# Optimization experiments

Measured on AMD Instinct MI355X. Metric: run time of the kernel, lower is better.

The kernel has to match this reference:

```python
import jax, jax.numpy as jnp
import numpy as np

B, CIN, H, W = 16, 3, 256, 256
COUT = 64
K = 3          # kernel size
PAD = 1
KK = K * K     # 9 taps
EPS = 1e-5     # BatchNorm eps


def conv3x3(x, w, b=None):
    y = jax.lax.conv_general_dilated(
        x, w, window_strides=(1, 1), padding=[(PAD, PAD), (PAD, PAD)],
        dimension_numbers=("NCHW", "OIHW", "NCHW"))
    if b is not None:
        y = y + b[None, :, None, None]
    return y


def deform_sample(x, off):
    """Bilinear sampling at per-pixel learned offsets (mmcv DeformConv2d, deform_groups=1).
    x: [B,C,H,W], off: [B,2*KK,H,W] interleaved (dy,dx) per kernel tap.
    Returns sampled taps [B,KK,H,W,C]."""
    b, c, h, w = x.shape
    dy = off[:, 0::2]  # [B,KK,H,W]
    dx = off[:, 1::2]
    ky, kx = jnp.meshgrid(jnp.arange(K), jnp.arange(K), indexing="ij")
    ky = (ky.reshape(-1) - PAD).astype(x.dtype)  # tap row offsets: -1,0,1
    kx = (kx.reshape(-1) - PAD).astype(x.dtype)
    gy = jnp.arange(h, dtype=x.dtype)
    gx = jnp.arange(w, dtype=x.dtype)
    # absolute (float) sampling positions per tap
    py = gy[None, None, :, None] + ky[None, :, None, None] + dy  # [B,KK,H,W]
    px = gx[None, None, None, :] + kx[None, :, None, None] + dx
    y0 = jnp.floor(py)
    x0 = jnp.floor(px)
    ly = py - y0
    lx = px - x0
    hy = 1.0 - ly
    hx = 1.0 - lx
    xt = x.transpose(0, 2, 3, 1)  # [B,H,W,C] for channel-last gather
    bi = jnp.arange(b)[:, None, None, None]

    def corner(yi, xi, wgt):
        valid = ((yi >= 0) & (yi <= h - 1) & (xi >= 0) & (xi <= w - 1)).astype(x.dtype)
        yc = jnp.clip(yi, 0, h - 1).astype(jnp.int32)
        xc = jnp.clip(xi, 0, w - 1).astype(jnp.int32)
        return xt[bi, yc, xc] * (wgt * valid)[..., None]  # [B,KK,H,W,C]

    v = (corner(y0, x0, hy * hx)
         + corner(y0, x0 + 1.0, hy * lx)
         + corner(y0 + 1.0, x0, ly * hx)
         + corner(y0 + 1.0, x0 + 1.0, ly * lx))
    return v


def setup_inputs() -> dict:
    key = jax.random.key(0)
    ks = jax.random.split(key, 7)
    x = jax.random.normal(ks[0], (B, CIN, H, W), dtype=jnp.float32)
    # conv_offset: 3x3 conv -> 2*KK offset channels (zero-init in mmcv; use small random)
    w_off = jax.random.normal(ks[1], (2 * KK, CIN, K, K), dtype=jnp.float32) * 0.01
    b_off = jnp.zeros((2 * KK,), dtype=jnp.float32)
    fan = CIN * KK
    w_dcn = jax.random.normal(ks[2], (COUT, CIN, K, K), dtype=jnp.float32) / np.sqrt(fan)
    w_conv = jax.random.normal(ks[3], (COUT, CIN, K, K), dtype=jnp.float32) / np.sqrt(fan)
    b_conv = jax.random.normal(ks[4], (COUT,), dtype=jnp.float32) * 0.01
    gamma = jnp.ones((COUT,), dtype=jnp.float32)
    beta = jnp.zeros((COUT,), dtype=jnp.float32)
    return {"x": x, "w_off": w_off, "b_off": b_off, "w_dcn": w_dcn,
            "w_conv": w_conv, "b_conv": b_conv, "gamma": gamma, "beta": beta}


def reference(x, w_off, b_off, w_dcn, w_conv, b_conv, gamma, beta):
    off = conv3x3(x, w_off, b_off)              # [B,18,H,W]
    taps = deform_sample(x, off)                # [B,KK,H,W,CIN]
    wk = w_dcn.reshape(COUT, CIN, KK).transpose(0, 2, 1)  # [O,KK,C]
    x_dcn = jnp.einsum("bkhwc,okc->bohw", taps, wk)       # deform conv (bias=False)
    x_res = conv3x3(x, w_conv, b_conv)
    y = x_res + x_dcn
    # BatchNorm2d (training mode: batch statistics, biased var)
    mean = y.mean(axis=(0, 2, 3))
    var = y.var(axis=(0, 2, 3))
    yn = (y - mean[None, :, None, None]) * jax.lax.rsqrt(var[None, :, None, None] + EPS)
    yb = yn * gamma[None, :, None, None] + beta[None, :, None, None]
    return yb * jax.nn.sigmoid(yb)  # SiLU
```

## Files before the change

kernel.cpp:

```cpp
#include <hip/hip_runtime.h>
#include <hip/hip_bf16.h>
#include <math.h>

#define BB 16
#define COUTC 64
#define HH 256
#define WWD 256
#define PW 260
#define NBLK (BB*HH)
#define NBLK2 2048
#define NBLKW (NBLK*4)
#define NPIX (BB*HH*WWD)
#define YTOT ((size_t)NPIX*COUTC)

typedef __attribute__((ext_vector_type(8))) short short8;
typedef __attribute__((ext_vector_type(4))) float f32x4;
typedef __attribute__((ext_vector_type(4))) unsigned short us4;
typedef __attribute__((ext_vector_type(8))) unsigned short us8;

__device__ __forceinline__ unsigned short f2bf(float f) {
    __hip_bfloat16 h = __float2bfloat16(f);
    return __builtin_bit_cast(unsigned short, h);
}
__device__ __forceinline__ float bf2f(unsigned short u) {
    unsigned v = (unsigned)u << 16;
    return __builtin_bit_cast(float, v);
}

__global__ __launch_bounds__(256) void prep_kernel(
    const float* __restrict__ x,
    us4* __restrict__ xp)
{
    const int b  = blockIdx.x / PW;
    const int yr = blockIdx.x % PW - 2;
    const bool rok = (yr >= 0) && (yr < HH);
    const float* xb = x + (size_t)b * (3*HH*WWD) + (size_t)(rok ? yr : 0)*WWD;
    for (int cx = threadIdx.x; cx < PW; cx += 256) {
        const int xx = cx - 2;
        const bool ok = rok && (xx >= 0) && (xx < WWD);
        float f0 = ok ? xb[0*(HH*WWD) + xx] : 0.f;
        float f1 = ok ? xb[1*(HH*WWD) + xx] : 0.f;
        float f2 = ok ? xb[2*(HH*WWD) + xx] : 0.f;
        us4 v = { f2bf(f0), f2bf(f1), f2bf(f2), 0 };
// ... 5 lines not shown
    const float* __restrict__ w_dcn,
    const float* __restrict__ w_conv,
    const float* __restrict__ w_off,
    unsigned short* __restrict__ wTg,
    unsigned short* __restrict__ wOg)
{
    for (int e = threadIdx.x; e < 512; e += 256) {
        const int kc = e >> 6, n = e & 63;
        const float* wsrc = (kc < 4) ? w_conv : w_dcn;
        const int kb = (kc & 3) * 8;
        us8 v;
        #pragma unroll
        for (int j = 0; j < 8; ++j) {
            int kk = kb + j;
            v[j] = (kk < 27) ? f2bf(wsrc[n*27 + kk]) : (unsigned short)0;
        }
        *(us8*)(wTg + e*8) = v;
    }
    if (threadIdx.x < 128) {
        const int e = threadIdx.x;
        const int nt2 = e >> 6, l = e & 63;
        const int n = nt2*16 + (l & 15);
        const int kb = (l >> 4) * 8;
        us8 v;
        #pragma unroll
        for (int j = 0; j < 8; ++j) {
            int kk = kb + j;
            v[j] = (n < 18 && kk < 27) ? f2bf(w_off[n*27 + kk]) : (unsigned short)0;
        }
        *(us8*)(wOg + e*8) = v;
    }
}

__device__ __forceinline__ void load_xn3(const us4* __restrict__ xpb, int h, int w,
                                         us8 r8[3], us4 r4[3])
{
    #pragma unroll
    for (int dy = 0; dy < 3; ++dy) {
        const us4* p = xpb + (size_t)(h+1+dy)*PW + (w+1);
        r8[dy] = *(const us8*)p;
        r4[dy] = p[2];
    }
}

template<bool BF16Y>
__global__ __launch_bounds__(256, 3) void dcn_wave_kernel(
    const float* __restrict__ x,
    const us4* __restrict__ xp,
    const unsigned short* __restrict__ wTg,
    const unsigned short* __restrict__ wOg,
    const float* __restrict__ b_off,
    const float* __restrict__ b_conv,
    float* __restrict__ outf,
    unsigned short* __restrict__ yws,
    float* __restrict__ psum,
    float* __restrict__ psq)
{
    __shared__ __align__(16) char kbuf[32768];
    __shared__ __align__(16) unsigned short sofs[4*64*24];

    const int tid = threadIdx.x;
    const int bid = blockIdx.x;
    const int w = tid;
    const int l   = tid & 63;
    const int wv  = tid >> 6;
    const int g   = l >> 4;
    const int r15 = l & 15;
    char* kw = kbuf + wv*8192;
    unsigned short* so = sofs + wv*64*24;

    short8 bfr[2][4];
    #pragma unroll
    for (int ks = 0; ks < 2; ++ks)
        #pragma unroll
        for (int nt = 0; nt < 4; ++nt) {
            const int kc = ks*4 + g, n = nt*16 + r15;
            bfr[ks][nt] = *(const short8*)(wTg + (kc*64 + n)*8);
        }
    short8 wof[2];
    #pragma unroll
    for (int nt2 = 0; nt2 < 2; ++nt2)
        wof[nt2] = *(const short8*)(wOg + (nt2*64 + l)*8);

    int eff = bid;
    int swz = ((eff & 7) << 9) | (eff >> 3);
    int b = swz >> 8, h = swz & 255;
    const us4* xpb = xp + (size_t)b*PW*PW;
    us8 c8v[3]; us4 c4v[3];
    load_xn3(xpb, h, w, c8v, c4v);

    #pragma unroll
    for (int it = 0; it < 2; ++it) {
        const int eff_n = eff + NBLK2;
        const int swz_n = ((eff_n & 7) << 9) | ((eff_n >> 3) & 511);
        const int b_n = swz_n >> 8, h_n = swz_n & 255;
        const us4* xpb_n = xp + (size_t)b_n*PW*PW;

        {
            unsigned short u[32];
            #pragma unroll
            for (int c = 0; c < 3; ++c)
                #pragma unroll
                for (int ky = 0; ky < 3; ++ky)
                    #pragma unroll
                    for (int kx = 0; kx < 3; ++kx)
                        u[c*9 + ky*3 + kx] = (kx == 2) ? c4v[ky][c]
                                                       : c8v[ky][kx*4 + c];
            #pragma unroll
            for (int k = 27; k < 32; ++k) u[k] = 0;
            #pragma unroll
            for (int c8 = 0; c8 < 4; ++c8) {
                uint4 v;
                v.x = (unsigned)u[c8*8+0] | ((unsigned)u[c8*8+1] << 16);
                v.y = (unsigned)u[c8*8+2] | ((unsigned)u[c8*8+3] << 16);
                v.z = (unsigned)u[c8*8+4] | ((unsigned)u[c8*8+5] << 16);
                v.w = (unsigned)u[c8*8+6] | ((unsigned)u[c8*8+7] << 16);
                *(uint4*)(kw + l*128 + ((c8 ^ (l & 7)) << 4)) = v;
            }
        }

        f32x4 dacc[4][2];
        {
            short8 af0[4];
            #pragma unroll
            for (int mt = 0; mt < 4; ++mt) {
                int row = mt*16 + r15;
                af0[mt] = *(const short8*)(kw + row*128 + ((g ^ (row & 7)) << 4));
            }
            #pragma unroll
            for (int mt = 0; mt < 4; ++mt)
                #pragma unroll
                for (int nt2 = 0; nt2 < 2; ++nt2) {
                    dacc[mt][nt2] = (f32x4){0.f, 0.f, 0.f, 0.f};
                    dacc[mt][nt2] = __builtin_amdgcn_mfma_f32_16x16x32_bf16(
                        af0[mt], wof[nt2], dacc[mt][nt2], 0, 0, 0);
                }
        }

        #pragma unroll
        for (int mt = 0; mt < 4; ++mt)
            #pragma unroll
            for (int nt2 = 0; nt2 < 2; ++nt2) {
                if (nt2 == 1 && r15 >= 2) continue;
                #pragma unroll
                for (int r = 0; r < 4; ++r)
                    so[(mt*16 + g*4 + r)*24 + nt2*16 + r15] = f2bf(dacc[mt][nt2][r]);
            }

        us8 n8[3]; us4 n4[3];
        if (it == 0) load_xn3(xpb_n, h_n, w, n8, n4);

        float off[18];
        {
            us8 o0 = *(const us8*)(so + l*24);
            us8 o1 = *(const us8*)(so + l*24 + 8);
            us4 o2 = *(const us4*)(so + l*24 + 16);
            #pragma unroll
            for (int j = 0; j < 8; ++j)  off[j]   = bf2f(o0[j]) + b_off[j];
            #pragma unroll
            for (int j = 0; j < 8; ++j)  off[8+j] = bf2f(o1[j]) + b_off[8+j];
            off[16] = bf2f(o2[0]) + b_off[16];
            off[17] = bf2f(o2[1]) + b_off[17];
        }

        unsigned short ut[32];
        #pragma unroll
        for (int k = 0; k < 9; ++k) {
            const int ky = k / 3, kx = k % 3;
            float py = (float)(h + ky - 1) + off[2*k];
            float px = (float)(w + kx - 1) + off[2*k + 1];
            float y0f = floorf(py), x0f = floorf(px);
            float ly = py - y0f, lx = px - x0f;
            float hy = 1.f - ly, hx = 1.f - lx;
            int y0 = (int)y0f, x0 = (int)x0f;
            float t0, t1, t2;

            if (__builtin_expect(y0 >= -2 && y0 <= 256 && x0 >= -2 && x0 <= 256, 1)) {
                const us4* p0 = xpb + (size_t)(y0+2)*PW + (x0+2);
                us8 r0 = *(const us8*)p0;
                us8 r1 = *(const us8*)(p0 + PW);
                float w00 = hy*hx, w01 = hy*lx, w10 = ly*hx, w11 = ly*lx;
                t0 = w00*bf2f(r0[0]) + w01*bf2f(r0[4]) + w10*bf2f(r1[0]) + w11*bf2f(r1[4]);
                t1 = w00*bf2f(r0[1]) + w01*bf2f(r0[5]) + w10*bf2f(r1[1]) + w11*bf2f(r1[5]);
                t2 = w00*bf2f(r0[2]) + w01*bf2f(r0[6]) + w10*bf2f(r1[2]) + w11*bf2f(r1[6]);
            } else {
                int y1 = y0 + 1, x1 = x0 + 1;
                bool vy0 = (y0 >= 0) && (y0 < HH);
                bool vy1 = (y1 >= 0) && (y1 < HH);
                bool vx0 = (x0 >= 0) && (x0 < WWD);
                bool vx1 = (x1 >= 0) && (x1 < WWD);
                float w00 = (vy0 && vx0) ? hy*hx : 0.f;
                float w01 = (vy0 && vx1) ? hy*lx : 0.f;
                float w10 = (vy1 && vx0) ? ly*hx : 0.f;
                float w11 = (vy1 && vx1) ? ly*lx : 0.f;
                int yc0 = min(max(y0, 0), HH-1),  yc1 = min(max(y1, 0), HH-1);
                int xc0 = min(max(x0, 0), WWD-1), xc1 = min(max(x1, 0), WWD-1);
                const float* xb = x + (size_t)b * (3*HH*WWD);
                const float* x0p = xb;
                t0 = w00*x0p[yc0*WWD+xc0] + w01*x0p[yc0*WWD+xc1]
                   + w10*x0p[yc1*WWD+xc0] + w11*x0p[yc1*WWD+xc1];
                const float* x1p = xb + HH*WWD;
                t1 = w00*x1p[yc0*WWD+xc0] + w01*x1p[yc0*WWD+xc1]
                   + w10*x1p[yc1*WWD+xc0] + w11*x1p[yc1*WWD+xc1];
                const float* x2p = xb + 2*HH*WWD;
                t2 = w00*x2p[yc0*WWD+xc0] + w01*x2p[yc0*WWD+xc1]
                   + w10*x2p[yc1*WWD+xc0] + w11*x2p[yc1*WWD+xc1];
            }
            ut[0*9 + k] = f2bf(t0);
            ut[1*9 + k] = f2bf(t1);
            ut[2*9 + k] = f2bf(t2);
        }
        #pragma unroll
        for (int k = 27; k < 32; ++k) ut[k] = 0;

        #pragma unroll
        for (int c8 = 4; c8 < 8; ++c8) {
            const int j0 = (c8 - 4) * 8;
            uint4 v;
            v.x = (unsigned)ut[j0+0] | ((unsigned)ut[j0+1] << 16);
            v.y = (unsigned)ut[j0+2] | ((unsigned)ut[j0+3] << 16);
            v.z = (unsigned)ut[j0+4] | ((unsigned)ut[j0+5] << 16);
            v.w = (unsigned)ut[j0+6] | ((unsigned)ut[j0+7] << 16);
            *(uint4*)(kw + l*128 + ((c8 ^ (l & 7)) << 4)) = v;
        }

        short8 a0[4], a1[4];
        #pragma unroll
        for (int mt = 0; mt < 4; ++mt) {
            int row = mt*16 + r15;
            a0[mt] = *(const short8*)(kw + row*128 + (( g      ^ (row & 7)) << 4));
            a1[mt] = *(const short8*)(kw + row*128 + (((4 + g) ^ (row & 7)) << 4));
        }

        #pragma unroll
        for (int nt = 0; nt < 4; ++nt) {
            f32x4 acc[4];
            #pragma unroll
            for (int mt = 0; mt < 4; ++mt)
                acc[mt] = (f32x4){0.f, 0.f, 0.f, 0.f};
            #pragma unroll
            for (int mt = 0; mt < 4; ++mt)
                acc[mt] = __builtin_amdgcn_mfma_f32_16x16x32_bf16(a0[mt], bfr[0][nt], acc[mt], 0, 0, 0);
            #pragma unroll
            for (int mt = 0; mt < 4; ++mt)
                acc[mt] = __builtin_amdgcn_mfma_f32_16x16x32_bf16(a1[mt], bfr[1][nt], acc[mt], 0, 0, 0);

            const float bcv = b_conv[nt*16 + r15];
            float s = 0.f, s2 = 0.f;
            const size_t base = ((size_t)(b*64 + nt*16 + r15) << 16)
                              + (size_t)h*256 + wv*64 + g*4;
            #pragma unroll
            for (int mt = 0; mt < 4; ++mt) {
                f32x4 v = acc[mt];
                float ox = v.x + bcv, oy = v.y + bcv, oz = v.z + bcv, ow = v.w + bcv;
                s += ox + oy + oz + ow;
                s2 = fmaf(ox, ox, s2); s2 = fmaf(oy, oy, s2);
                s2 = fmaf(oz, oz, s2); s2 = fmaf(ow, ow, s2);
                if (BF16Y) {
                    us4 pv = { f2bf(ox), f2bf(oy), f2bf(oz), f2bf(ow) };
                    *(us4*)(yws + base + mt*16) = pv;
                } else {
                    float4 pv = { ox, oy, oz, ow };
                    *(float4*)(outf + base + mt*16) = pv;
                }
            }
            s  += __shfl_xor(s, 16);  s  += __shfl_xor(s, 32);
            s2 += __shfl_xor(s2, 16); s2 += __shfl_xor(s2, 32);
            if (l < 16) {
                psum[(nt*16 + l)*NBLKW + swz*4 + wv] = s;
                psq [(nt*16 + l)*NBLKW + swz*4 + wv] = s2;
            }
        }

        if (it == 0) {
            eff = eff_n; swz = swz_n; b = b_n; h = h_n; xpb = xpb_n;
            #pragma unroll
            for (int dy = 0; dy < 3; ++dy) { c8v[dy] = n8[dy]; c4v[dy] = n4[dy]; }
        }
    }
}

__global__ __launch_bounds__(256) void bn_stats_kernel(
    const float* __restrict__ psum,
    const float* __restrict__ psq,
    const float* __restrict__ gamma,
    const float* __restrict__ beta,
    float* __restrict__ ss)
{
    __shared__ float rs[256], rq[256];
    const int ch = blockIdx.x, tid = threadIdx.x;
    float s = 0.f, s2 = 0.f;
    for (int j = tid; j < NBLKW; j += 256) {
        s  += psum[ch*NBLKW + j];
        s2 += psq [ch*NBLKW + j];
    }
    rs[tid] = s; rq[tid] = s2;
    __syncthreads();
    for (int st = 128; st > 0; st >>= 1) {
        if (tid < st) { rs[tid] += rs[tid + st]; rq[tid] += rq[tid + st]; }
        __syncthreads();
    }
    if (tid == 0) {
        const float N = (float)NPIX;
        float mean = rs[0] / N;
        float var  = rq[0] / N - mean*mean;
        float rstd = rsqrtf(var + 1e-5f);
        float sc   = gamma[ch] * rstd;
        ss[ch]      = sc;
        ss[64 + ch] = beta[ch] - mean * sc;
    }
}

// ... 49 lines not shown
        z = fmaf(v.w, a, t); v.w = z / (1.f + __expf(-z));
        y4[i] = v;
    }
}

extern "C" void kernel_launch(void* const* d_in, const int* in_sizes, int n_in,
                              void* d_out, int out_size, void* d_ws, size_t ws_size,
                              hipStream_t stream) {
    const float* x      = (const float*)d_in[0];
    const float* w_off  = (const float*)d_in[1];
    const float* b_off  = (const float*)d_in[2];
    const float* w_dcn  = (const float*)d_in[3];
    const float* w_conv = (const float*)d_in[4];
    const float* b_conv = (const float*)d_in[5];
    const float* gamma  = (const float*)d_in[6];
    const float* beta   = (const float*)d_in[7];
    float* out = (float*)d_out;

    const size_t yBytes    = YTOT * 2;
    const size_t xpBytes   = (size_t)BB*PW*PW*8;
    const size_t wtgBytes  = 8192 + 2048;
    const size_t statBytes = 2*(size_t)64*NBLKW*4 + 512;

    if (ws_size >= yBytes + xpBytes + wtgBytes + statBytes) {
        unsigned short* yws = (unsigned short*)d_ws;
        us4*            xpp = (us4*)((char*)d_ws + yBytes);
        unsigned short* wTg = (unsigned short*)((char*)d_ws + yBytes + xpBytes);
        unsigned short* wOg = wTg + 4096;
        float* psum = (float*)((char*)d_ws + yBytes + xpBytes + wtgBytes);
        float* psq  = psum + (size_t)64*NBLKW;
        float* ss   = psq  + (size_t)64*NBLKW;
        prep_kernel<<<BB*PW, 256, 0, stream>>>(x, xpp);
        wtg_kernel<<<1, 256, 0, stream>>>(w_dcn, w_conv, w_off, wTg, wOg);
        dcn_wave_kernel<true><<<NBLK2, 256, 0, stream>>>(
            x, xpp, wTg, wOg, b_off, b_conv, nullptr, yws, psum, psq);
        bn_stats_kernel<<<64, 256, 0, stream>>>(psum, psq, gamma, beta, ss);
        bn_silu_bf16_kernel<<<2048, 256, 0, stream>>>(yws, out, ss);
    } else {
        us4*            xpp = (us4*)d_ws;
        unsigned short* wTg = (unsigned short*)((char*)d_ws + xpBytes);
        unsigned short* wOg = wTg + 4096;
        float* psum = (float*)((char*)d_ws + xpBytes + wtgBytes);
        float* psq  = psum + (size_t)64*NBLKW;
        float* ss   = psq  + (size_t)64*NBLKW;
        prep_kernel<<<BB*PW, 256, 0, stream>>>(x, xpp);
        wtg_kernel<<<1, 256, 0, stream>>>(w_dcn, w_conv, w_off, wTg, wOg);
        dcn_wave_kernel<false><<<NBLK2, 256, 0, stream>>>(
            x, xpp, wTg, wOg, b_off, b_conv, out, nullptr, psum, psq);
        bn_stats_kernel<<<64, 256, 0, stream>>>(psum, psq, gamma, beta, ss);
        bn_silu_kernel<<<2048, 256, 0, stream>>>(out, ss);
    }
}
```

Baseline: 184.8 us.

## Batch all deformable tap gathers upfront, one row per block, drop fp32 fallback

The kernel now handles one image row per block over NBLK blocks, replacing the two-row loop that software-prefetched the next row's neighbourhood. It first computes offsets, weights and clamped addresses for all nine taps, then issues all eighteen gathers together so they are in flight at once. The out-of-window fallback now reads the padded bf16 buffer instead of the fp32 input, and index maths uses 32-bit unsigned arithmetic. Launch bounds drop from 3 to 2 blocks per SU, trading occupancy and extra registers for more memory-level parallelism per thread.

New measurement: 187.8 us. Within noise of the previous version (+1.6%).

```diff
diff --git a/kernel.cpp b/kernel.cpp
--- a/kernel.cpp
+++ b/kernel.cpp
@@ -8,7 +8,6 @@
 #define WWD 256
 #define PW 260
 #define NBLK (BB*HH)
-#define NBLK2 2048
 #define NBLKW (NBLK*4)
 #define NPIX (BB*HH*WWD)
 #define YTOT ((size_t)NPIX*COUTC)
@@ -80,20 +79,8 @@
     }
 }
 
-__device__ __forceinline__ void load_xn3(const us4* __restrict__ xpb, int h, int w,
-                                         us8 r8[3], us4 r4[3])
-{
-    #pragma unroll
-    for (int dy = 0; dy < 3; ++dy) {
-        const us4* p = xpb + (size_t)(h+1+dy)*PW + (w+1);
-        r8[dy] = *(const us8*)p;
-        r4[dy] = p[2];
-    }
-}
-
 template<bool BF16Y>
-__global__ __launch_bounds__(256, 3) void dcn_wave_kernel(
-    const float* __restrict__ x,
+__global__ __launch_bounds__(256, 2) void dcn_wave_kernel(
     const us4* __restrict__ xp,
     const unsigned short* __restrict__ wTg,
     const unsigned short* __restrict__ wOg,
@@ -109,6 +96,9 @@
 
     const int tid = threadIdx.x;
     const int bid = blockIdx.x;
+    const int swz = ((bid & 7) << 9) | (bid >> 3);
+    const int b = swz >> 8;
+    const int h = swz & 255;
     const int w = tid;
     const int l   = tid & 63;
     const int wv  = tid >> 6;
@@ -117,6 +107,16 @@
     char* kw = kbuf + wv*8192;
     unsigned short* so = sofs + wv*64*24;
 
+    const us4* xpb = xp + (unsigned)b*(PW*PW);
+
+    us8 c8v[3]; us4 c4v[3];
+    #pragma unroll
+    for (int dy = 0; dy < 3; ++dy) {
+        const us4* p = xpb + (unsigned)((h+1+dy)*PW + (w+1));
+        c8v[dy] = *(const us8*)p;
+        c4v[dy] = p[2];
+    }
+
     short8 bfr[2][4];
     #pragma unroll
     for (int ks = 0; ks < 2; ++ks)
@@ -130,108 +130,116 @@
     for (int nt2 = 0; nt2 < 2; ++nt2)
         wof[nt2] = *(const short8*)(wOg + (nt2*64 + l)*8);
 
-    int eff = bid;
-    int swz = ((eff & 7) << 9) | (eff >> 3);
-    int b = swz >> 8, h = swz & 255;
-    const us4* xpb = xp + (size_t)b*PW*PW;
-    us8 c8v[3]; us4 c4v[3];
-    load_xn3(xpb, h, w, c8v, c4v);
-
-    #pragma unroll
-    for (int it = 0; it < 2; ++it) {
-        const int eff_n = eff + NBLK2;
-        const int swz_n = ((eff_n & 7) << 9) | ((eff_n >> 3) & 511);
-        const int b_n = swz_n >> 8, h_n = swz_n & 255;
-        const us4* xpb_n = xp + (size_t)b_n*PW*PW;
-
-        {
-            unsigned short u[32];
+    {
+        unsigned short u[32];
+        #pragma unroll
+        for (int c = 0; c < 3; ++c)
             #pragma unroll
-            for (int c = 0; c < 3; ++c)
+            for (int ky = 0; ky < 3; ++ky)
                 #pragma unroll
-                for (int ky = 0; ky < 3; ++ky)
-                    #pragma unroll
-                    for (int kx = 0; kx < 3; ++kx)
-                        u[c*9 + ky*3 + kx] = (kx == 2) ? c4v[ky][c]
-                                                       : c8v[ky][kx*4 + c];
-            #pragma unroll
-            for (int k = 27; k < 32; ++k) u[k] = 0;
-            #pragma unroll
-            for (int c8 = 0; c8 < 4; ++c8) {
-                uint4 v;
-                v.x = (unsigned)u[c8*8+0] | ((unsigned)u[c8*8+1] << 16);
-                v.y = (unsigned)u[c8*8+2] | ((unsigned)u[c8*8+3] << 16);
-                v.z = (unsigned)u[c8*8+4] | ((unsigned)u[c8*8+5] << 16);
-                v.w = (unsigned)u[c8*8+6] | ((unsigned)u[c8*8+7] << 16);
-                *(uint4*)(kw + l*128 + ((c8 ^ (l & 7)) << 4)) = v;
-            }
-        }
-
-        f32x4 dacc[4][2];
-        {
-            short8 af0[4];
-            #pragma unroll
-            for (int mt = 0; mt < 4; ++mt) {
-                int row = mt*16 + r15;
-                af0[mt] = *(const short8*)(kw + row*128 + ((g ^ (row & 7)) << 4));
-            }
-            #pragma unroll
-            for (int mt = 0; mt < 4; ++mt)
-                #pragma unroll
-                for (int nt2 = 0; nt2 < 2; ++nt2) {
-                    dacc[mt][nt2] = (f32x4){0.f, 0.f, 0.f, 0.f};
-                    dacc[mt][nt2] = __builtin_amdgcn_mfma_f32_16x16x32_bf16(
-                        af0[mt], wof[nt2], dacc[mt][nt2], 0, 0, 0);
-                }
-        }
-
+                for (int kx = 0; kx < 3; ++kx)
+                    u[c*9 + ky*3 + kx] = (kx == 2) ? c4v[ky][c]
+                                                   : c8v[ky][kx*4 + c];
+        #pragma unroll
+        for (int k = 27; k < 32; ++k) u[k] = 0;
+        #pragma unroll
+        for (int c8 = 0; c8 < 4; ++c8) {
+            uint4 v;
+            v.x = (unsigned)u[c8*8+0] | ((unsigned)u[c8*8+1] << 16);
+            v.y = (unsigned)u[c8*8+2] | ((unsigned)u[c8*8+3] << 16);
+            v.z = (unsigned)u[c8*8+4] | ((unsigned)u[c8*8+5] << 16);
+            v.w = (unsigned)u[c8*8+6] | ((unsigned)u[c8*8+7] << 16);
+            *(uint4*)(kw + l*128 + ((c8 ^ (l & 7)) << 4)) = v;
+        }
+    }
+
+    f32x4 dacc[4][2];
+    {
+        short8 af0[4];
+        #pragma unroll
+        for (int mt = 0; mt < 4; ++mt) {
+            int row = mt*16 + r15;
+            af0[mt] = *(const short8*)(kw + row*128 + ((g ^ (row & 7)) << 4));
+        }
         #pragma unroll
         for (int mt = 0; mt < 4; ++mt)
             #pragma unroll
             for (int nt2 = 0; nt2 < 2; ++nt2) {
-                if (nt2 == 1 && r15 >= 2) continue;
-                #pragma unroll
-                for (int r = 0; r < 4; ++r)
-                    so[(mt*16 + g*4 + r)*24 + nt2*16 + r15] = f2bf(dacc[mt][nt2][r]);
+                dacc[mt][nt2] = (f32x4){0.f, 0.f, 0.f, 0.f};
+                dacc[mt][nt2] = __builtin_amdgcn_mfma_f32_16x16x32_bf16(
+                    af0[mt], wof[nt2], dacc[mt][nt2], 0, 0, 0);
             }
-
-        us8 n8[3]; us4 n4[3];
-        if (it == 0) load_xn3(xpb_n, h_n, w, n8, n4);
-
-        float off[18];
-        {
-            us8 o0 = *(const us8*)(so + l*24);
-            us8 o1 = *(const us8*)(so + l*24 + 8);
-            us4 o2 = *(const us4*)(so + l*24 + 16);
+    }
+
+    #pragma unroll
+    for (int mt = 0; mt < 4; ++mt)
+        #pragma unroll
+        for (int nt2 = 0; nt2 < 2; ++nt2) {
+            if (nt2 == 1 && r15 >= 2) continue;
             #pragma unroll
-            for (int j = 0; j < 8; ++j)  off[j]   = bf2f(o0[j]) + b_off[j];
-            #pragma unroll
-            for (int j = 0; j < 8; ++j)  off[8+j] = bf2f(o1[j]) + b_off[8+j];
-            off[16] = bf2f(o2[0]) + b_off[16];
-            off[17] = bf2f(o2[1]) + b_off[17];
-        }
-
-        unsigned short ut[32];
-        #pragma unroll
-        for (int k = 0; k < 9; ++k) {
-            const int ky = k / 3, kx = k % 3;
-            float py = (float)(h + ky - 1) + off[2*k];
-            float px = (float)(w + kx - 1) + off[2*k + 1];
-            float y0f = floorf(py), x0f = floorf(px);
-            float ly = py - y0f, lx = px - x0f;
-            float hy = 1.f - ly, hx = 1.f - lx;
-            int y0 = (int)y0f, x0 = (int)x0f;
-            float t0, t1, t2;
-
-            if (__builtin_expect(y0 >= -2 && y0 <= 256 && x0 >= -2 && x0 <= 256, 1)) {
-                const us4* p0 = xpb + (size_t)(y0+2)*PW + (x0+2);
-                us8 r0 = *(const us8*)p0;
-                us8 r1 = *(const us8*)(p0 + PW);
-                float w00 = hy*hx, w01 = hy*lx, w10 = ly*hx, w11 = ly*lx;
-                t0 = w00*bf2f(r0[0]) + w01*bf2f(r0[4]) + w10*bf2f(r1[0]) + w11*bf2f(r1[4]);
-                t1 = w00*bf2f(r0[1]) + w01*bf2f(r0[5]) + w10*bf2f(r1[1]) + w11*bf2f(r1[5]);
-                t2 = w00*bf2f(r0[2]) + w01*bf2f(r0[6]) + w10*bf2f(r1[2]) + w11*bf2f(r1[6]);
-            } else {
+            for (int r = 0; r < 4; ++r)
+                so[(mt*16 + g*4 + r)*24 + nt2*16 + r15] = f2bf(dacc[mt][nt2][r]);
+        }
+
+    float off[18];
+    {
+        us8 o0 = *(const us8*)(so + l*24);
+        us8 o1 = *(const us8*)(so + l*24 + 8);
+        us4 o2 = *(const us4*)(so + l*24 + 16);
+        #pragma unroll
+        for (int j = 0; j < 8; ++j)  off[j]   = bf2f(o0[j]) + b_off[j];
+        #pragma unroll
+        for (int j = 0; j < 8; ++j)  off[8+j] = bf2f(o1[j]) + b_off[8+j];
+        off[16] = bf2f(o2[0]) + b_off[16];
+        off[17] = bf2f(o2[1]) + b_off[17];
+    }
+
+    int   o32[9];
+    float W00[9], W01[9], W10[9], W11[9];
+    unsigned inwm = 0;
+    #pragma unroll
+    for (int k = 0; k < 9; ++k) {
+        const int ky = k / 3, kx = k % 3;
+        float py = (float)(h + ky - 1) + off[2*k];
+        float px = (float)(w + kx - 1) + off[2*k + 1];
+        float y0f = floorf(py), x0f = floorf(px);
+        float ly = py - y0f, lx = px - x0f;
+        float hy = 1.f - ly, hx = 1.f - lx;
+        int y0 = (int)y0f, x0 = (int)x0f;
+        bool inw = (y0 >= -2) & (y0 <= 256) & (x0 >= -2) & (x0 <= 256);
+        inwm |= (unsigned)inw << k;
+        int y0c = min(max(y0, -2), 256), x0c = min(max(x0, -2), 256);
+        o32[k] = (y0c + 2)*PW + (x0c + 2);
+        W00[k] = hy*hx; W01[k] = hy*lx; W10[k] = ly*hx; W11[k] = ly*lx;
+    }
+
+    us8 ra[9], rb[9];
+    #pragma unroll
+    for (int k = 0; k < 9; ++k) {
+        const us4* p0 = xpb + (unsigned)o32[k];
+        ra[k] = *(const us8*)p0;
+        rb[k] = *(const us8*)(p0 + PW);
+    }
+
+    unsigned short ut[32];
+    #pragma unroll
+    for (int k = 0; k < 9; ++k) {
+        float t0 = W00[k]*bf2f(ra[k][0]) + W01[k]*bf2f(ra[k][4])
+                 + W10[k]*bf2f(rb[k][0]) + W11[k]*bf2f(rb[k][4]);
+        float t1 = W00[k]*bf2f(ra[k][1]) + W01[k]*bf2f(ra[k][5])
+                 + W10[k]*bf2f(rb[k][1]) + W11[k]*bf2f(rb[k][5]);
+        float t2 = W00[k]*bf2f(ra[k][2]) + W01[k]*bf2f(ra[k][6])
+                 + W10[k]*bf2f(rb[k][2]) + W11[k]*bf2f(rb[k][6]);
+
+        if (__builtin_expect(__any(((inwm >> k) & 1u) == 0u), 0)) {
+            if (!((inwm >> k) & 1u)) {
+                const int ky = k / 3, kx = k % 3;
+                float py = (float)(h + ky - 1) + off[2*k];
+                float px = (float)(w + kx - 1) + off[2*k + 1];
+                float y0f = floorf(py), x0f = floorf(px);
+                float ly = py - y0f, lx = px - x0f;
+                float hy = 1.f - ly, hx = 1.f - lx;
+                int y0 = (int)y0f, x0 = (int)x0f;
                 int y1 = y0 + 1, x1 = x0 + 1;
                 bool vy0 = (y0 >= 0) && (y0 < HH);
                 bool vy1 = (y1 >= 0) && (y1 < HH);
@@ -243,87 +251,78 @@
                 float w11 = (vy1 && vx1) ? ly*lx : 0.f;
                 int yc0 = min(max(y0, 0), HH-1),  yc1 = min(max(y1, 0), HH-1);
                 int xc0 = min(max(x0, 0), WWD-1), xc1 = min(max(x1, 0), WWD-1);
-                const float* xb = x + (size_t)b * (3*HH*WWD);
-                const float* x0p = xb;
-                t0 = w00*x0p[yc0*WWD+xc0] + w01*x0p[yc0*WWD+xc1]
-                   + w10*x0p[yc1*WWD+xc0] + w11*x0p[yc1*WWD+xc1];
-                const float* x1p = xb + HH*WWD;
-                t1 = w00*x1p[yc0*WWD+xc0] + w01*x1p[yc0*WWD+xc1]
-                   + w10*x1p[yc1*WWD+xc0] + w11*x1p[yc1*WWD+xc1];
-                const float* x2p = xb + 2*HH*WWD;
-                t2 = w00*x2p[yc0*WWD+xc0] + w01*x2p[yc0*WWD+xc1]
-                   + w10*x2p[yc1*WWD+xc0] + w11*x2p[yc1*WWD+xc1];
+                us4 q00 = xpb[(unsigned)((yc0+2)*PW + xc0+2)];
+                us4 q01 = xpb[(unsigned)((yc0+2)*PW + xc1+2)];
+                us4 q10 = xpb[(unsigned)((yc1+2)*PW + xc0+2)];
+                us4 q11 = xpb[(unsigned)((yc1+2)*PW + xc1+2)];
+                t0 = w00*bf2f(q00[0]) + w01*bf2f(q01[0]) + w10*bf2f(q10[0]) + w11*bf2f(q11[0]);
+                t1 = w00*bf2f(q00[1]) + w01*bf2f(q01[1]) + w10*bf2f(q10[1]) + w11*bf2f(q11[1]);
+                t2 = w00*bf2f(q00[2]) + w01*bf2f(q01[2]) + w10*bf2f(q10[2]) + w11*bf2f(q11[2]);
             }
-            ut[0*9 + k] = f2bf(t0);
-            ut[1*9 + k] = f2bf(t1);
-            ut[2*9 + k] = f2bf(t2);
-        }
-        #pragma unroll
-        for (int k = 27; k < 32; ++k) ut[k] = 0;
-
-        #pragma unroll
-        for (int c8 = 4; c8 < 8; ++c8) {
-            const int j0 = (c8 - 4) * 8;
-            uint4 v;
-            v.x = (unsigned)ut[j0+0] | ((unsigned)ut[j0+1] << 16);
-            v.y = (unsigned)ut[j0+2] | ((unsigned)ut[j0+3] << 16);
-            v.z = (unsigned)ut[j0+4] | ((unsigned)ut[j0+5] << 16);
-            v.w = (unsigned)ut[j0+6] | ((unsigned)ut[j0+7] << 16);
-            *(uint4*)(kw + l*128 + ((c8 ^ (l & 7)) << 4)) = v;
-        }
-
-        short8 a0[4], a1[4];
+        }
+        ut[0*9 + k] = f2bf(t0);
+        ut[1*9 + k] = f2bf(t1);
+        ut[2*9 + k] = f2bf(t2);
+    }
+    #pragma unroll
+    for (int k = 27; k < 32; ++k) ut[k] = 0;
+
+    #pragma unroll
+    for (int c8 = 4; c8 < 8; ++c8) {
+        const int j0 = (c8 - 4) * 8;
+        uint4 v;
+        v.x = (unsigned)ut[j0+0] | ((unsigned)ut[j0+1] << 16);
+        v.y = (unsigned)ut[j0+2] | ((unsigned)ut[j0+3] << 16);
+        v.z = (unsigned)ut[j0+4] | ((unsigned)ut[j0+5] << 16);
+        v.w = (unsigned)ut[j0+6] | ((unsigned)ut[j0+7] << 16);
+        *(uint4*)(kw + l*128 + ((c8 ^ (l & 7)) << 4)) = v;
+    }
+
+    short8 a0[4], a1[4];
+    #pragma unroll
+    for (int mt = 0; mt < 4; ++mt) {
+        int row = mt*16 + r15;
+        a0[mt] = *(const short8*)(kw + row*128 + (( g      ^ (row & 7)) << 4));
+        a1[mt] = *(const short8*)(kw + row*128 + (((4 + g) ^ (row & 7)) << 4));
+    }
+
+    #pragma unroll
+    for (int nt = 0; nt < 4; ++nt) {
+        f32x4 acc[4];
+        #pragma unroll
+        for (int mt = 0; mt < 4; ++mt)
+            acc[mt] = (f32x4){0.f, 0.f, 0.f, 0.f};
+        #pragma unroll
+        for (int mt = 0; mt < 4; ++mt)
+            acc[mt] = __builtin_amdgcn_mfma_f32_16x16x32_bf16(a0[mt], bfr[0][nt], acc[mt], 0, 0, 0);
+        #pragma unroll
+        for (int mt = 0; mt < 4; ++mt)
+            acc[mt] = __builtin_amdgcn_mfma_f32_16x16x32_bf16(a1[mt], bfr[1][nt], acc[mt], 0, 0, 0);
+
+        const float bcv = b_conv[nt*16 + r15];
+        float s = 0.f, s2 = 0.f;
+        const unsigned base = ((unsigned)(b*64 + nt*16 + r15) << 16)
+                            + (unsigned)(h*256 + wv*64 + g*4);
         #pragma unroll
         for (int mt = 0; mt < 4; ++mt) {
-            int row = mt*16 + r15;
-            a0[mt] = *(const short8*)(kw + row*128 + (( g      ^ (row & 7)) << 4));
-            a1[mt] = *(const short8*)(kw + row*128 + (((4 + g) ^ (row & 7)) << 4));
-        }
-
-        #pragma unroll
-        for (int nt = 0; nt < 4; ++nt) {
-            f32x4 acc[4];
-            #pragma unroll
-            for (int mt = 0; mt < 4; ++mt)
-                acc[mt] = (f32x4){0.f, 0.f, 0.f, 0.f};
-            #pragma unroll
-            for (int mt = 0; mt < 4; ++mt)
-                acc[mt] = __builtin_amdgcn_mfma_f32_16x16x32_bf16(a0[mt], bfr[0][nt], acc[mt], 0, 0, 0);
-            #pragma unroll
-            for (int mt = 0; mt < 4; ++mt)
-                acc[mt] = __builtin_amdgcn_mfma_f32_16x16x32_bf16(a1[mt], bfr[1][nt], acc[mt], 0, 0, 0);
-
-            const float bcv = b_conv[nt*16 + r15];
-            float s = 0.f, s2 = 0.f;
-            const size_t base = ((size_t)(b*64 + nt*16 + r15) << 16)
-                              + (size_t)h*256 + wv*64 + g*4;
-            #pragma unroll
-            for (int mt = 0; mt < 4; ++mt) {
-                f32x4 v = acc[mt];
-                float ox = v.x + bcv, oy = v.y + bcv, oz = v.z + bcv, ow = v.w + bcv;
-                s += ox + oy + oz + ow;
-                s2 = fmaf(ox, ox, s2); s2 = fmaf(oy, oy, s2);
-                s2 = fmaf(oz, oz, s2); s2 = fmaf(ow, ow, s2);
-                if (BF16Y) {
-                    us4 pv = { f2bf(ox), f2bf(oy), f2bf(oz), f2bf(ow) };
-                    *(us4*)(yws + base + mt*16) = pv;
-                } else {
-                    float4 pv = { ox, oy, oz, ow };
-                    *(float4*)(outf + base + mt*16) = pv;
-                }
+            f32x4 v = acc[mt];
+            float ox = v.x + bcv, oy = v.y + bcv, oz = v.z + bcv, ow = v.w + bcv;
+            s += ox + oy + oz + ow;
+            s2 = fmaf(ox, ox, s2); s2 = fmaf(oy, oy, s2);
+            s2 = fmaf(oz, oz, s2); s2 = fmaf(ow, ow, s2);
+            if (BF16Y) {
+                us4 pv = { f2bf(ox), f2bf(oy), f2bf(oz), f2bf(ow) };
+                *(us4*)(yws + base + mt*16) = pv;
+            } else {
+                float4 pv = { ox, oy, oz, ow };
+                *(float4*)(outf + base + mt*16) = pv;
             }
-            s  += __shfl_xor(s, 16);  s  += __shfl_xor(s, 32);
-            s2 += __shfl_xor(s2, 16); s2 += __shfl_xor(s2, 32);
-            if (l < 16) {
-                psum[(nt*16 + l)*NBLKW + swz*4 + wv] = s;
-                psq [(nt*16 + l)*NBLKW + swz*4 + wv] = s2;
-            }
-        }
-
-        if (it == 0) {
-            eff = eff_n; swz = swz_n; b = b_n; h = h_n; xpb = xpb_n;
-            #pragma unroll
-            for (int dy = 0; dy < 3; ++dy) { c8v[dy] = n8[dy]; c4v[dy] = n4[dy]; }
+        }
+        s  += __shfl_xor(s, 16);  s  += __shfl_xor(s, 32);
+        s2 += __shfl_xor(s2, 16); s2 += __shfl_xor(s2, 32);
+        if (l < 16) {
+            psum[(unsigned)((nt*16 + l)*NBLKW + swz*4 + wv)] = s;
+            psq [(unsigned)((nt*16 + l)*NBLKW + swz*4 + wv)] = s2;
         }
     }
 }
@@ -441,8 +440,8 @@
         float* ss   = psq  + (size_t)64*NBLKW;
         prep_kernel<<<BB*PW, 256, 0, stream>>>(x, xpp);
         wtg_kernel<<<1, 256, 0, stream>>>(w_dcn, w_conv, w_off, wTg, wOg);
-        dcn_wave_kernel<true><<<NBLK2, 256, 0, stream>>>(
-            x, xpp, wTg, wOg, b_off, b_conv, nullptr, yws, psum, psq);
+        dcn_wave_kernel<true><<<NBLK, 256, 0, stream>>>(
+            xpp, wTg, wOg, b_off, b_conv, nullptr, yws, psum, psq);
         bn_stats_kernel<<<64, 256, 0, stream>>>(psum, psq, gamma, beta, ss);
         bn_silu_bf16_kernel<<<2048, 256, 0, stream>>>(yws, out, ss);
     } else {
@@ -454,8 +453,8 @@
         float* ss   = psq  + (size_t)64*NBLKW;
         prep_kernel<<<BB*PW, 256, 0, stream>>>(x, xpp);
         wtg_kernel<<<1, 256, 0, stream>>>(w_dcn, w_conv, w_off, wTg, wOg);
-        dcn_wave_kernel<false><<<NBLK2, 256, 0, stream>>>(
-            x, xpp, wTg, wOg, b_off, b_conv, out, nullptr, psum, psq);
+        dcn_wave_kernel<false><<<NBLK, 256, 0, stream>>>(
+            xpp, wTg, wOg, b_off, b_conv, out, nullptr, psum, psq);
         bn_stats_kernel<<<64, 256, 0, stream>>>(psum, psq, gamma, beta, ss);
         bn_silu_kernel<<<2048, 256, 0, stream>>>(out, ss);
     }
```

## Software-pipeline two row tiles per block with interleaved gather loads

Applied to the files above, without the earlier changes.

Restructures the deform-conv kernel so each block processes its two rows in an interleaved schedule. Both rows' offset convs run first, then the second row's gather loads are issued while the first row's bilinear math and main MFMA run. This hides global gather latency. The out-of-bounds fallback that read unpadded x is replaced by clamping coordinates into the padded buffer, and 32-bit offsets replace size_t addressing. LDS doubles and launch bounds drop to 2 blocks per CU to make room for the extra live state, which costs occupancy.

New measurement: 181.7 us. Within noise of the previous version (-1.7%).

```diff
diff --git a/kernel.cpp b/kernel.cpp
--- a/kernel.cpp
+++ b/kernel.cpp
@@ -85,15 +85,197 @@
 {
     #pragma unroll
     for (int dy = 0; dy < 3; ++dy) {
-        const us4* p = xpb + (size_t)(h+1+dy)*PW + (w+1);
+        const us4* p = xpb + (unsigned)((h+1+dy)*PW + (w+1));
         r8[dy] = *(const us8*)p;
         r4[dy] = p[2];
     }
 }
 
+__device__ __forceinline__ void pack_xn_half(char* kw, int l,
+                                             const us8 c8v[3], const us4 c4v[3])
+{
+    unsigned short u[32];
+    #pragma unroll
+    for (int c = 0; c < 3; ++c)
+        #pragma unroll
+        for (int ky = 0; ky < 3; ++ky)
+            #pragma unroll
+            for (int kx = 0; kx < 3; ++kx)
+                u[c*9 + ky*3 + kx] = (kx == 2) ? c4v[ky][c] : c8v[ky][kx*4 + c];
+    #pragma unroll
+    for (int k = 27; k < 32; ++k) u[k] = 0;
+    #pragma unroll
+    for (int c8 = 0; c8 < 4; ++c8) {
+        uint4 v;
+        v.x = (unsigned)u[c8*8+0] | ((unsigned)u[c8*8+1] << 16);
+        v.y = (unsigned)u[c8*8+2] | ((unsigned)u[c8*8+3] << 16);
+        v.z = (unsigned)u[c8*8+4] | ((unsigned)u[c8*8+5] << 16);
+        v.w = (unsigned)u[c8*8+6] | ((unsigned)u[c8*8+7] << 16);
+        *(uint4*)(kw + l*128 + ((c8 ^ (l & 7)) << 4)) = v;
+    }
+}
+
+__device__ __forceinline__ void off_conv_mfma(const char* kw, int g, int r15,
+                                              const short8 wof[2], f32x4 dacc[4][2])
+{
+    short8 af0[4];
+    #pragma unroll
+    for (int mt = 0; mt < 4; ++mt) {
+        int row = mt*16 + r15;
+        af0[mt] = *(const short8*)(kw + row*128 + ((g ^ (row & 7)) << 4));
+    }
+    #pragma unroll
+    for (int mt = 0; mt < 4; ++mt)
+        #pragma unroll
+        for (int nt2 = 0; nt2 < 2; ++nt2) {
+            dacc[mt][nt2] = (f32x4){0.f, 0.f, 0.f, 0.f};
+            dacc[mt][nt2] = __builtin_amdgcn_mfma_f32_16x16x32_bf16(
+                af0[mt], wof[nt2], dacc[mt][nt2], 0, 0, 0);
+        }
+}
+
+__device__ __forceinline__ void redist_read_off(unsigned short* so, int l, int g,
+                                                int r15, const f32x4 dacc[4][2],
+                                                const float* __restrict__ b_off,
+                                                float off[18])
+{
+    #pragma unroll
+    for (int mt = 0; mt < 4; ++mt)
+        #pragma unroll
+        for (int nt2 = 0; nt2 < 2; ++nt2) {
+            if (nt2 == 1 && r15 >= 2) continue;
+            #pragma unroll
+            for (int r = 0; r < 4; ++r)
+                so[(mt*16 + g*4 + r)*24 + nt2*16 + r15] = f2bf(dacc[mt][nt2][r]);
+        }
+    us8 o0 = *(const us8*)(so + l*24);
+    us8 o1 = *(const us8*)(so + l*24 + 8);
+    us4 o2 = *(const us4*)(so + l*24 + 16);
+    #pragma unroll
+    for (int j = 0; j < 8; ++j)  off[j]   = bf2f(o0[j]) + b_off[j];
+    #pragma unroll
+    for (int j = 0; j < 8; ++j)  off[8+j] = bf2f(o1[j]) + b_off[8+j];
+    off[16] = bf2f(o2[0]) + b_off[16];
+    off[17] = bf2f(o2[1]) + b_off[17];
+}
+
+__device__ __forceinline__ void tap_addrs(int h, int w, const float off[18],
+                                          int o32[9], float W00[9], float W01[9],
+                                          float W10[9], float W11[9])
+{
+    #pragma unroll
+    for (int k = 0; k < 9; ++k) {
+        const int ky = k / 3, kx = k % 3;
+        float py = (float)(h + ky - 1) + off[2*k];
+        float px = (float)(w + kx - 1) + off[2*k + 1];
+        float y0f = floorf(py), x0f = floorf(px);
+        float ly = py - y0f, lx = px - x0f;
+        float hy = 1.f - ly, hx = 1.f - lx;
+        int y0 = min(max((int)y0f, -2), 256);
+        int x0 = min(max((int)x0f, -2), 256);
+        o32[k] = (y0 + 2)*PW + (x0 + 2);
+        W00[k] = hy*hx; W01[k] = hy*lx; W10[k] = ly*hx; W11[k] = ly*lx;
+    }
+}
+
+__device__ __forceinline__ void tap_loads(const us4* __restrict__ xpb,
+                                          const int o32[9], us8 ra[9], us8 rb[9])
+{
+    #pragma unroll
+    for (int k = 0; k < 9; ++k) {
+        const us4* p0 = xpb + (unsigned)o32[k];
+        ra[k] = *(const us8*)p0;
+        rb[k] = *(const us8*)(p0 + PW);
+    }
+}
+
+__device__ __forceinline__ void tap_math_pack(char* kw, int l,
+                                              const float W00[9], const float W01[9],
+                                              const float W10[9], const float W11[9],
+                                              const us8 ra[9], const us8 rb[9])
+{
+    unsigned short ut[32];
+    #pragma unroll
+    for (int k = 0; k < 9; ++k) {
+        #pragma unroll
+        for (int c = 0; c < 3; ++c) {
+            float t = W00[k]*bf2f(ra[k][c])   + W01[k]*bf2f(ra[k][4+c])
+                    + W10[k]*bf2f(rb[k][c])   + W11[k]*bf2f(rb[k][4+c]);
+            ut[c*9 + k] = f2bf(t);
+        }
+    }
+    #pragma unroll
+    for (int k = 27; k < 32; ++k) ut[k] = 0;
+    #pragma unroll
+    for (int c8 = 4; c8 < 8; ++c8) {
+        const int j0 = (c8 - 4) * 8;
+        uint4 v;
+        v.x = (unsigned)ut[j0+0] | ((unsigned)ut[j0+1] << 16);
+        v.y = (unsigned)ut[j0+2] | ((unsigned)ut[j0+3] << 16);
+        v.z = (unsigned)ut[j0+4] | ((unsigned)ut[j0+5] << 16);
+        v.w = (unsigned)ut[j0+6] | ((unsigned)ut[j0+7] << 16);
+        *(uint4*)(kw + l*128 + ((c8 ^ (l & 7)) << 4)) = v;
+    }
+}
+
 template<bool BF16Y>
-__global__ __launch_bounds__(256, 3) void dcn_wave_kernel(
-    const float* __restrict__ x,
+__device__ __forceinline__ void main_mfma_epilogue(
+    const char* kw, int l, int wv, int g, int r15,
+    const short8 bfr[2][4], const float* __restrict__ b_conv,
+    int swz, int b, int h,
+    float* __restrict__ outf, unsigned short* __restrict__ yws,
+    float* __restrict__ psum, float* __restrict__ psq)
+{
+    short8 a0[4], a1[4];
+    #pragma unroll
+    for (int mt = 0; mt < 4; ++mt) {
+        int row = mt*16 + r15;
+        a0[mt] = *(const short8*)(kw + row*128 + (( g      ^ (row & 7)) << 4));
+        a1[mt] = *(const short8*)(kw + row*128 + (((4 + g) ^ (row & 7)) << 4));
+    }
+    #pragma unroll
+    for (int nt = 0; nt < 4; ++nt) {
+        f32x4 acc[4];
+        #pragma unroll
+        for (int mt = 0; mt < 4; ++mt)
+            acc[mt] = (f32x4){0.f, 0.f, 0.f, 0.f};
+        #pragma unroll
+        for (int mt = 0; mt < 4; ++mt)
+            acc[mt] = __builtin_amdgcn_mfma_f32_16x16x32_bf16(a0[mt], bfr[0][nt], acc[mt], 0, 0, 0);
+        #pragma unroll
+        for (int mt = 0; mt < 4; ++mt)
+            acc[mt] = __builtin_amdgcn_mfma_f32_16x16x32_bf16(a1[mt], bfr[1][nt], acc[mt], 0, 0, 0);
+
+        const float bcv = b_conv[nt*16 + r15];
+        float s = 0.f, s2 = 0.f;
+        const size_t base = ((size_t)(b*64 + nt*16 + r15) << 16)
+                          + (size_t)h*256 + wv*64 + g*4;
+        #pragma unroll
+        for (int mt = 0; mt < 4; ++mt) {
+            f32x4 v = acc[mt];
+            float ox = v.x + bcv, oy = v.y + bcv, oz = v.z + bcv, ow = v.w + bcv;
+            s += ox + oy + oz + ow;
+            s2 = fmaf(ox, ox, s2); s2 = fmaf(oy, oy, s2);
+            s2 = fmaf(oz, oz, s2); s2 = fmaf(ow, ow, s2);
+            if (BF16Y) {
+                us4 pv = { f2bf(ox), f2bf(oy), f2bf(oz), f2bf(ow) };
+                *(us4*)(yws + base + mt*16) = pv;
+            } else {
+                float4 pv = { ox, oy, oz, ow };
+                *(float4*)(outf + base + mt*16) = pv;
+            }
+        }
+        s  += __shfl_xor(s, 16);  s  += __shfl_xor(s, 32);
+        s2 += __shfl_xor(s2, 16); s2 += __shfl_xor(s2, 32);
+        if (l < 16) {
+            psum[(nt*16 + l)*NBLKW + swz*4 + wv] = s;
+            psq [(nt*16 + l)*NBLKW + swz*4 + wv] = s2;
+        }
+    }
+}
+
+template<bool BF16Y>
+__global__ __launch_bounds__(256, 2) void dcn_wave_kernel(
     const us4* __restrict__ xp,
     const unsigned short* __restrict__ wTg,
     const unsigned short* __restrict__ wOg,
@@ -104,8 +286,8 @@
     float* __restrict__ psum,
     float* __restrict__ psq)
 {
-    __shared__ __align__(16) char kbuf[32768];
-    __shared__ __align__(16) unsigned short sofs[4*64*24];
+    __shared__ __align__(16) char kbuf[65536];
+    __shared__ __align__(16) unsigned short sofs[6144];
 
     const int tid = threadIdx.x;
     const int bid = blockIdx.x;
@@ -114,8 +296,17 @@
     const int wv  = tid >> 6;
     const int g   = l >> 4;
     const int r15 = l & 15;
-    char* kw = kbuf + wv*8192;
+    char* kw0 = kbuf + wv*8192;
+    char* kw1 = kbuf + (4 + wv)*8192;
     unsigned short* so = sofs + wv*64*24;
+
+    const int eff0 = bid,         eff1 = bid + NBLK2;
+    const int swz0 = ((eff0 & 7) << 9) | (eff0 >> 3);
+    const int swz1 = ((eff1 & 7) << 9) | ((eff1 >> 3) & 511);
+    const int b0 = swz0 >> 8, h0 = swz0 & 255;
+    const int b1 = swz1 >> 8, h1 = swz1 & 255;
+    const us4* xpb0 = xp + (size_t)b0*PW*PW;
+    const us4* xpb1 = xp + (size_t)b1*PW*PW;
 
     short8 bfr[2][4];
     #pragma unroll
@@ -130,202 +321,41 @@
     for (int nt2 = 0; nt2 < 2; ++nt2)
         wof[nt2] = *(const short8*)(wOg + (nt2*64 + l)*8);
 
-    int eff = bid;
-    int swz = ((eff & 7) << 9) | (eff >> 3);
-    int b = swz >> 8, h = swz & 255;
-    const us4* xpb = xp + (size_t)b*PW*PW;
-    us8 c8v[3]; us4 c4v[3];
-    load_xn3(xpb, h, w, c8v, c4v);
-
-    #pragma unroll
-    for (int it = 0; it < 2; ++it) {
-        const int eff_n = eff + NBLK2;
-        const int swz_n = ((eff_n & 7) << 9) | ((eff_n >> 3) & 511);
-        const int b_n = swz_n >> 8, h_n = swz_n & 255;
-        const us4* xpb_n = xp + (size_t)b_n*PW*PW;
-
-        {
-            unsigned short u[32];
-            #pragma unroll
-            for (int c = 0; c < 3; ++c)
-                #pragma unroll
-                for (int ky = 0; ky < 3; ++ky)
-                    #pragma unroll
-                    for (int kx = 0; kx < 3; ++kx)
-                        u[c*9 + ky*3 + kx] = (kx == 2) ? c4v[ky][c]
-                                                       : c8v[ky][kx*4 + c];
-            #pragma unroll
-            for (int k = 27; k < 32; ++k) u[k] = 0;
-            #pragma unroll
-            for (int c8 = 0; c8 < 4; ++c8) {
-                uint4 v;
-                v.x = (unsigned)u[c8*8+0] | ((unsigned)u[c8*8+1] << 16);
-                v.y = (unsigned)u[c8*8+2] | ((unsigned)u[c8*8+3] << 16);
-                v.z = (unsigned)u[c8*8+4] | ((unsigned)u[c8*8+5] << 16);
-                v.w = (unsigned)u[c8*8+6] | ((unsigned)u[c8*8+7] << 16);
-                *(uint4*)(kw + l*128 + ((c8 ^ (l & 7)) << 4)) = v;
-            }
-        }
-
-        f32x4 dacc[4][2];
-        {
-            short8 af0[4];
-            #pragma unroll
-            for (int mt = 0; mt < 4; ++mt) {
-                int row = mt*16 + r15;
-                af0[mt] = *(const short8*)(kw + row*128 + ((g ^ (row & 7)) << 4));
-            }
-            #pragma unroll
-            for (int mt = 0; mt < 4; ++mt)
-                #pragma unroll
-                for (int nt2 = 0; nt2 < 2; ++nt2) {
-                    dacc[mt][nt2] = (f32x4){0.f, 0.f, 0.f, 0.f};
-                    dacc[mt][nt2] = __builtin_amdgcn_mfma_f32_16x16x32_bf16(
-                        af0[mt], wof[nt2], dacc[mt][nt2], 0, 0, 0);
-                }
-        }
-
-        #pragma unroll
-        for (int mt = 0; mt < 4; ++mt)
-            #pragma unroll
-            for (int nt2 = 0; nt2 < 2; ++nt2) {
-                if (nt2 == 1 && r15 >= 2) continue;
-                #pragma unroll
-                for (int r = 0; r < 4; ++r)
-                    so[(mt*16 + g*4 + r)*24 + nt2*16 + r15] = f2bf(dacc[mt][nt2][r]);
-            }
-
-        us8 n8[3]; us4 n4[3];
-        if (it == 0) load_xn3(xpb_n, h_n, w, n8, n4);
-
-        float off[18];
-        {
-            us8 o0 = *(const us8*)(so + l*24);
-            us8 o1 = *(const us8*)(so + l*24 + 8);
-            us4 o2 = *(const us4*)(so + l*24 + 16);
-            #pragma unroll
-            for (int j = 0; j < 8; ++j)  off[j]   = bf2f(o0[j]) + b_off[j];
-            #pragma unroll
-            for (int j = 0; j < 8; ++j)  off[8+j] = bf2f(o1[j]) + b_off[8+j];
-            off[16] = bf2f(o2[0]) + b_off[16];
-            off[17] = bf2f(o2[1]) + b_off[17];
-        }
-
-        unsigned short ut[32];
-        #pragma unroll
-        for (int k = 0; k < 9; ++k) {
-            const int ky = k / 3, kx = k % 3;
-            float py = (float)(h + ky - 1) + off[2*k];
-            float px = (float)(w + kx - 1) + off[2*k + 1];
-            float y0f = floorf(py), x0f = floorf(px);
-            float ly = py - y0f, lx = px - x0f;
-            float hy = 1.f - ly, hx = 1.f - lx;
-            int y0 = (int)y0f, x0 = (int)x0f;
-            float t0, t1, t2;
-
-            if (__builtin_expect(y0 >= -2 && y0 <= 256 && x0 >= -2 && x0 <= 256, 1)) {
-                const us4* p0 = xpb + (size_t)(y0+2)*PW + (x0+2);
-                us8 r0 = *(const us8*)p0;
-                us8 r1 = *(const us8*)(p0 + PW);
-                float w00 = hy*hx, w01 = hy*lx, w10 = ly*hx, w11 = ly*lx;
-                t0 = w00*bf2f(r0[0]) + w01*bf2f(r0[4]) + w10*bf2f(r1[0]) + w11*bf2f(r1[4]);
-                t1 = w00*bf2f(r0[1]) + w01*bf2f(r0[5]) + w10*bf2f(r1[1]) + w11*bf2f(r1[5]);
-                t2 = w00*bf2f(r0[2]) + w01*bf2f(r0[6]) + w10*bf2f(r1[2]) + w11*bf2f(r1[6]);
-            } else {
-                int y1 = y0 + 1, x1 = x0 + 1;
-                bool vy0 = (y0 >= 0) && (y0 < HH);
-                bool vy1 = (y1 >= 0) && (y1 < HH);
-                bool vx0 = (x0 >= 0) && (x0 < WWD);
-                bool vx1 = (x1 >= 0) && (x1 < WWD);
-                float w00 = (vy0 && vx0) ? hy*hx : 0.f;
-                float w01 = (vy0 && vx1) ? hy*lx : 0.f;
-                float w10 = (vy1 && vx0) ? ly*hx : 0.f;
-                float w11 = (vy1 && vx1) ? ly*lx : 0.f;
-                int yc0 = min(max(y0, 0), HH-1),  yc1 = min(max(y1, 0), HH-1);
-                int xc0 = min(max(x0, 0), WWD-1), xc1 = min(max(x1, 0), WWD-1);
-                const float* xb = x + (size_t)b * (3*HH*WWD);
-                const float* x0p = xb;
-                t0 = w00*x0p[yc0*WWD+xc0] + w01*x0p[yc0*WWD+xc1]
-                   + w10*x0p[yc1*WWD+xc0] + w11*x0p[yc1*WWD+xc1];
-                const float* x1p = xb + HH*WWD;
-                t1 = w00*x1p[yc0*WWD+xc0] + w01*x1p[yc0*WWD+xc1]
-                   + w10*x1p[yc1*WWD+xc0] + w11*x1p[yc1*WWD+xc1];
-                const float* x2p = xb + 2*HH*WWD;
-                t2 = w00*x2p[yc0*WWD+xc0] + w01*x2p[yc0*WWD+xc1]
-                   + w10*x2p[yc1*WWD+xc0] + w11*x2p[yc1*WWD+xc1];
-            }
-            ut[0*9 + k] = f2bf(t0);
-            ut[1*9 + k] = f2bf(t1);
-            ut[2*9 + k] = f2bf(t2);
-        }
-        #pragma unroll
-        for (int k = 27; k < 32; ++k) ut[k] = 0;
-
-        #pragma unroll
-        for (int c8 = 4; c8 < 8; ++c8) {
-            const int j0 = (c8 - 4) * 8;
-            uint4 v;
-            v.x = (unsigned)ut[j0+0] | ((unsigned)ut[j0+1] << 16);
-            v.y = (unsigned)ut[j0+2] | ((unsigned)ut[j0+3] << 16);
-            v.z = (unsigned)ut[j0+4] | ((unsigned)ut[j0+5] << 16);
-            v.w = (unsigned)ut[j0+6] | ((unsigned)ut[j0+7] << 16);
-            *(uint4*)(kw + l*128 + ((c8 ^ (l & 7)) << 4)) = v;
-        }
-
-        short8 a0[4], a1[4];
-        #pragma unroll
-        for (int mt = 0; mt < 4; ++mt) {
-            int row = mt*16 + r15;
-            a0[mt] = *(const short8*)(kw + row*128 + (( g      ^ (row & 7)) << 4));
-            a1[mt] = *(const short8*)(kw + row*128 + (((4 + g) ^ (row & 7)) << 4));
-        }
-
-        #pragma unroll
-        for (int nt = 0; nt < 4; ++nt) {
-            f32x4 acc[4];
-            #pragma unroll
-            for (int mt = 0; mt < 4; ++mt)
-                acc[mt] = (f32x4){0.f, 0.f, 0.f, 0.f};
-            #pragma unroll
-            for (int mt = 0; mt < 4; ++mt)
-                acc[mt] = __builtin_amdgcn_mfma_f32_16x16x32_bf16(a0[mt], bfr[0][nt], acc[mt], 0, 0, 0);
-            #pragma unroll
-            for (int mt = 0; mt < 4; ++mt)
-                acc[mt] = __builtin_amdgcn_mfma_f32_16x16x32_bf16(a1[mt], bfr[1][nt], acc[mt], 0, 0, 0);
-
-            const float bcv = b_conv[nt*16 + r15];
-            float s = 0.f, s2 = 0.f;
-            const size_t base = ((size_t)(b*64 + nt*16 + r15) << 16)
-                              + (size_t)h*256 + wv*64 + g*4;
-            #pragma unroll
-            for (int mt = 0; mt < 4; ++mt) {
-                f32x4 v = acc[mt];
-                float ox = v.x + bcv, oy = v.y + bcv, oz = v.z + bcv, ow = v.w + bcv;
-                s += ox + oy + oz + ow;
-                s2 = fmaf(ox, ox, s2); s2 = fmaf(oy, oy, s2);
-                s2 = fmaf(oz, oz, s2); s2 = fmaf(ow, ow, s2);
-                if (BF16Y) {
-                    us4 pv = { f2bf(ox), f2bf(oy), f2bf(oz), f2bf(ow) };
-                    *(us4*)(yws + base + mt*16) = pv;
-                } else {
-                    float4 pv = { ox, oy, oz, ow };
-                    *(float4*)(outf + base + mt*16) = pv;
-                }
-            }
-            s  += __shfl_xor(s, 16);  s  += __shfl_xor(s, 32);
-            s2 += __shfl_xor(s2, 16); s2 += __shfl_xor(s2, 32);
-            if (l < 16) {
-                psum[(nt*16 + l)*NBLKW + swz*4 + wv] = s;
-                psq [(nt*16 + l)*NBLKW + swz*4 + wv] = s2;
-            }
-        }
-
-        if (it == 0) {
-            eff = eff_n; swz = swz_n; b = b_n; h = h_n; xpb = xpb_n;
-            #pragma unroll
-            for (int dy = 0; dy < 3; ++dy) { c8v[dy] = n8[dy]; c4v[dy] = n4[dy]; }
-        }
-    }
+    us8 c8v0[3]; us4 c4v0[3];
+    us8 c8v1[3]; us4 c4v1[3];
+    load_xn3(xpb0, h0, w, c8v0, c4v0);
+    load_xn3(xpb1, h1, w, c8v1, c4v1);
+
+    pack_xn_half(kw0, l, c8v0, c4v0);
+    pack_xn_half(kw1, l, c8v1, c4v1);
+
+    f32x4 dacc0[4][2], dacc1[4][2];
+    off_conv_mfma(kw0, g, r15, wof, dacc0);
+    off_conv_mfma(kw1, g, r15, wof, dacc1);
+
+    float off0[18], off1[18];
+    redist_read_off(so, l, g, r15, dacc0, b_off, off0);
+    redist_read_off(so, l, g, r15, dacc1, b_off, off1);
+
+    int o32_0[9]; float W00_0[9], W01_0[9], W10_0[9], W11_0[9];
+    tap_addrs(h0, w, off0, o32_0, W00_0, W01_0, W10_0, W11_0);
+    us8 ra0[9], rb0[9];
+    tap_loads(xpb0, o32_0, ra0, rb0);
+
+    int o32_1[9]; float W00_1[9], W01_1[9], W10_1[9], W11_1[9];
+    tap_addrs(h1, w, off1, o32_1, W00_1, W01_1, W10_1, W11_1);
+
+    tap_math_pack(kw0, l, W00_0, W01_0, W10_0, W11_0, ra0, rb0);
+
+    us8 ra1[9], rb1[9];
+    tap_loads(xpb1, o32_1, ra1, rb1);
+
+    main_mfma_epilogue<BF16Y>(kw0, l, wv, g, r15, bfr, b_conv,
+                              swz0, b0, h0, outf, yws, psum, psq);
+
+    tap_math_pack(kw1, l, W00_1, W01_1, W10_1, W11_1, ra1, rb1);
+    main_mfma_epilogue<BF16Y>(kw1, l, wv, g, r15, bfr, b_conv,
+                              swz1, b1, h1, outf, yws, psum, psq);
 }
 
 __global__ __launch_bounds__(256) void bn_stats_kernel(
@@ -442,7 +472,7 @@
         prep_kernel<<<BB*PW, 256, 0, stream>>>(x, xpp);
         wtg_kernel<<<1, 256, 0, stream>>>(w_dcn, w_conv, w_off, wTg, wOg);
         dcn_wave_kernel<true><<<NBLK2, 256, 0, stream>>>(
-            x, xpp, wTg, wOg, b_off, b_conv, nullptr, yws, psum, psq);
+            xpp, wTg, wOg, b_off, b_conv, nullptr, yws, psum, psq);
         bn_stats_kernel<<<64, 256, 0, stream>>>(psum, psq, gamma, beta, ss);
         bn_silu_bf16_kernel<<<2048, 256, 0, stream>>>(yws, out, ss);
     } else {
@@ -455,7 +485,7 @@
         prep_kernel<<<BB*PW, 256, 0, stream>>>(x, xpp);
         wtg_kernel<<<1, 256, 0, stream>>>(w_dcn, w_conv, w_off, wTg, wOg);
         dcn_wave_kernel<false><<<NBLK2, 256, 0, stream>>>(
-            x, xpp, wTg, wOg, b_off, b_conv, out, nullptr, psum, psq);
+            xpp, wTg, wOg, b_off, b_conv, out, nullptr, psum, psq);
         bn_stats_kernel<<<64, 256, 0, stream>>>(psum, psq, gamma, beta, ss);
         bn_silu_kernel<<<2048, 256, 0, stream>>>(out, ss);
     }
```
